# Kernel optimization log

Hardware: AMD Instinct MI355X
Metric: run time of the kernel (lower is better)

## Reference

```python
import jax, jax.numpy as jnp
import numpy as np

NEG_INF = -1.0e9
LEAKY_SLOPE = 0.2


def setup_inputs() -> dict:
    key = jax.random.key(0)
    ks = jax.random.split(key, 8)
    B, H, N, D = 4, 8, 256, 64
    query = jax.random.normal(ks[0], (B, H, N, D), dtype=jnp.float32)
    k_ = jax.random.normal(ks[1], (B, H, N, D), dtype=jnp.float32)
    value = jax.random.normal(ks[2], (B, H, N, D), dtype=jnp.float32)
    mask = jax.random.randint(ks[3], (B, 1, N, N), 0, 2, dtype=jnp.int32)
    # nn.Linear(d_k*2, d_k): weight (D, 2D), bias (D,)
    lim_h = 1.0 / np.sqrt(2 * D)
    W_h = jax.random.uniform(ks[4], (D, 2 * D), minval=-lim_h, maxval=lim_h, dtype=jnp.float32)
    b_h = jax.random.uniform(ks[5], (D,), minval=-lim_h, maxval=lim_h, dtype=jnp.float32)
    # nn.Linear(d_k, 1): weight (1, D), bias (1,)
    lim_o = 1.0 / np.sqrt(D)
    W_o = jax.random.uniform(ks[6], (1, D), minval=-lim_o, maxval=lim_o, dtype=jnp.float32)
    b_o = jax.random.uniform(ks[7], (1,), minval=-lim_o, maxval=lim_o, dtype=jnp.float32)
    return {"query": query, "key": k_, "value": value, "mask": mask,
            "W_h": W_h, "b_h": b_h, "W_o": W_o, "b_o": b_o}


def reference(query, key, value, mask, W_h, b_h, W_o, b_o):
    # W_h acts on concat([q, k]); decompose into two projections (same math):
    # W_h @ [q; k] = q @ W_q^T + k @ W_k^T
    D = query.shape[-1]
    Wq, Wk = W_h[:, :D], W_h[:, D:]
    q_proj = jnp.einsum('bhnd,ed->bhne', query, Wq)  # (B,H,N,D)
    k_proj = jnp.einsum('bhmd,ed->bhme', key, Wk)    # (B,H,N,D)
    # pairwise hidden: (B,H,N,N,D)
    hidden = q_proj[:, :, :, None, :] + k_proj[:, :, None, :, :] + b_h
    hidden = jax.nn.leaky_relu(hidden, negative_slope=LEAKY_SLOPE)
    scores = jnp.einsum('bhnme,e->bhnm', hidden, W_o[0]) + b_o[0]  # (B,H,N,N)
    scores = jnp.where(mask == 0, NEG_INF, scores)
    p_attn = jax.nn.softmax(scores, axis=-1)
    out = jnp.einsum('bhnm,bhmd->bhnd', p_attn, value)
    return out, p_attn
```

## Files before the change

kernel.cpp:

```cpp
#include <hip/hip_runtime.h>

constexpr int B = 4, H = 8, N = 256, D = 64;
constexpr int QBLK = 8;
constexpr int PATTN_OFF = B * H * N * D;
constexpr int NROWS = B * H * N;


__global__ __launch_bounds__(256) void proj_kernel(
    const float* __restrict__ q, const float* __restrict__ k,
    const float* __restrict__ W_h, const float* __restrict__ b_h,
    const float* __restrict__ W_o, const float* __restrict__ b_o,
    float* __restrict__ qp, float* __restrict__ kpb,
    float* __restrict__ cq6, float* __restrict__ ck6, float* __restrict__ w4)
{
    __shared__ float WT[128 * 65];
    int t = threadIdx.x;
    int lane = t & 63;
    int wid = __builtin_amdgcn_readfirstlane(t >> 6);
    int bid = blockIdx.x;
    int work = (bid & 7) * 32 + (bid >> 3);

    #pragma unroll
    for (int i = 0; i < 8; ++i) {
        int fidx = (t + i * 256) * 4;
        float4 w = *reinterpret_cast<const float4*>(W_h + fidx);
        int e = fidx >> 7, d = fidx & 127;
        WT[(d + 0) * 65 + e] = w.x;
        WT[(d + 1) * 65 + e] = w.y;
        WT[(d + 2) * 65 + e] = w.z;
        WT[(d + 3) * 65 + e] = w.w;
    }
    if (bid == 0 && t < 64) w4[t] = 0.4f * W_o[t];
    __syncthreads();

    int rbase = work * 32 + wid * 8;
    float accq[8] = {}, acck[8] = {};
    #pragma unroll
    for (int d0 = 0; d0 < 64; d0 += 16) {
        float wq[16], wk[16];
        #pragma unroll
        for (int d = 0; d < 16; ++d) {
            wq[d] = WT[(d0 + d) * 65 + lane];
            wk[d] = WT[(64 + d0 + d) * 65 + lane];
        }
        #pragma unroll
        for (int j = 0; j < 8; ++j) {
            const float* qrow = q + (rbase + j) * 64 + d0;
            const float* krow = k + (rbase + j) * 64 + d0;
            #pragma unroll
            for (int d = 0; d < 16; ++d) {
                accq[j] = fmaf(qrow[d], wq[d], accq[j]);
                acck[j] = fmaf(krow[d], wk[d], acck[j]);
            }
        }
    }
    float bh_e = b_h[lane];
    float wo = W_o[lane];
    float bo = b_o[0];
    #pragma unroll
    for (int j = 0; j < 8; ++j) {
        float aq = accq[j];
        float ak = acck[j] + bh_e;
        qp[(rbase + j) * 64 + lane] = aq;
        kpb[(rbase + j) * 64 + lane] = ak;
        float sq = wo * aq, sk = wo * ak;
        #pragma unroll
        for (int off = 32; off > 0; off >>= 1) {
            sq += __shfl_xor(sq, off, 64);
            sk += __shfl_xor(sk, off, 64);
        }
        if (lane == 0) {
            cq6[rbase + j] = 0.6f * sq + bo;
            ck6[rbase + j] = 0.6f * sk;
        }
    }
}

__global__ __launch_bounds__(512, 2) void attn_kernel(
    const float* __restrict__ qp, const float* __restrict__ kpb,
    const float* __restrict__ V, const int* __restrict__ mask,
    const float* __restrict__ cq6, const float* __restrict__ ck6,
    const float* __restrict__ w4g,
    float* __restrict__ out)
{
    __shared__ float smem[6144];
    __shared__ float red_s[8][4];

    int t = threadIdx.x;
    int lane = t & 63;
    int wid = __builtin_amdgcn_readfirstlane(t >> 6);
    int h = wid >> 2;
    int m = t & 255;
    int bid = blockIdx.x;
    int work = (bid & 7) * 128 + (bid >> 3);
    int bh = work >> 5;
    int nb = work & 31;
    int b = bh >> 3;
    int n0 = nb * QBLK;
    int kvbase = bh * N * 64;

    const float4* kp4 = reinterpret_cast<const float4*>(kpb + kvbase + m * 64 + h * 32);
    float4 c0 = kp4[0], c1 = kp4[1];

    float mf[4];
    #pragma unroll
    for (int i = 0; i < 4; ++i)
        mf[i] = (mask[(b * N + n0 + h * 4 + i) * N + m] != 0) ? 1.0f : 0.0f;

    float ckt = (h == 0) ? ck6[bh * N + m] : 0.f;

    float sp[8];
    const float* cq = cq6 + bh * N + n0;
    #pragma unroll
    for (int r = 0; r < 8; ++r) sp[r] = (h == 0) ? (cq[r] + ckt) : 0.f;

    const float* qr  = qp + (bh * N + n0) * 64 + h * 32;
    const float* w4h = w4g + h * 32;
    #pragma unroll
    for (int chunk = 0; chunk < 4; ++chunk) {
        float4 p0, p1;
        if (chunk < 3) { p0 = kp4[2 * chunk + 2]; p1 = kp4[2 * chunk + 3]; }
        float kvv[8] = {c0.x, c0.y, c0.z, c0.w, c1.x, c1.y, c1.z, c1.w};
        const float* qrc = qr + chunk * 8;
        const float* w4c = w4h + chunk * 8;
        #pragma unroll
        for (int e1 = 0; e1 < 8; ++e1) {
            float kve = kvv[e1];
            float we = w4c[e1];
            #pragma unroll
            for (int r = 0; r < 8; ++r)
                sp[r] = fmaf(we, fabsf(qrc[r * 64 + e1] + kve), sp[r]);
        }
        c0 = p0; c1 = p1;
    }
    #pragma unroll
    for (int r = 0; r < 8; ++r)
        smem[h * 2048 + r * 256 + m] = sp[r];

    const float* Vp = V + kvbase + wid * 32 * 64 + lane;
    float vpre0 = Vp[0 * 64], vpre1 = Vp[1 * 64], vpre2 = Vp[2 * 64], vpre3 = Vp[3 * 64];
    __syncthreads();

    float p8[4];
    #pragma unroll
    for (int i = 0; i < 4; ++i) {
        int rr = h * 4 + i;
        float s = smem[rr * 256 + m] + smem[2048 + rr * 256 + m];
        float p = __expf(s) * mf[i];
        p8[i] = p;
        float l = p;
        #pragma unroll
        for (int off = 32; off > 0; off >>= 1) l += __shfl_xor(l, off, 64);
        if (lane == 0) red_s[wid][i] = l;
    }
    __syncthreads();

    #pragma unroll
    for (int i = 0; i < 4; ++i) {
        int rr = h * 4 + i;
        float gs = red_s[h*4+0][i] + red_s[h*4+1][i] + red_s[h*4+2][i] + red_s[h*4+3][i];
        float pn = p8[i] * __frcp_rn(gs);
        smem[rr * 256 + m] = pn;
        out[PATTN_OFF + (bh * N + n0 + rr) * N + m] = pn;
    }
    __syncthreads();

    float acc[8] = {};
    {
        #pragma unroll
        for (int r = 0; r < 8; ++r) {
            float4 p4 = *reinterpret_cast<const float4*>(&smem[r * 256 + wid * 32]);
            acc[r] = fmaf(p4.x, vpre0, fmaf(p4.y, vpre1, fmaf(p4.z, vpre2, fmaf(p4.w, vpre3, acc[r]))));
        }
    }
    #pragma unroll
    for (int j = 4; j < 32; j += 4) {
        float v0 = Vp[(j+0) * 64];
        float v1 = Vp[(j+1) * 64];
        float v2 = Vp[(j+2) * 64];
        float v3 = Vp[(j+3) * 64];
        #pragma unroll
        for (int r = 0; r < 8; ++r) {
            float4 p4 = *reinterpret_cast<const float4*>(&smem[r * 256 + wid * 32 + j]);
            acc[r] = fmaf(p4.x, v0, fmaf(p4.y, v1, fmaf(p4.z, v2, fmaf(p4.w, v3, acc[r]))));
        }
    }
    #pragma unroll
    for (int r = 0; r < 8; ++r)
        smem[2048 + wid * 512 + r * 64 + lane] = acc[r];
    __syncthreads();

    float o = 0.f;
    #pragma unroll
    for (int mc = 0; mc < 8; ++mc)
        o += smem[2048 + mc * 512 + wid * 64 + lane];
    out[(bh * N + n0 + wid) * 64 + lane] = o;
}

extern "C" void kernel_launch(void* const* d_in, const int* in_sizes, int n_in,
                              void* d_out, int out_size, void* d_ws, size_t ws_size,
                              hipStream_t stream) {
    const float* q    = (const float*)d_in[0];
    const float* k    = (const float*)d_in[1];
    const float* v    = (const float*)d_in[2];
    const int*   mask = (const int*)d_in[3];
    const float* W_h  = (const float*)d_in[4];
    const float* b_h  = (const float*)d_in[5];
    const float* W_o  = (const float*)d_in[6];
    const float* b_o  = (const float*)d_in[7];
    float* out = (float*)d_out;

    float* qp  = (float*)d_ws;
    float* kpb = qp + NROWS * 64;
    float* cq6 = kpb + NROWS * 64;
    float* ck6 = cq6 + NROWS;
    float* w4  = ck6 + NROWS;

    proj_kernel<<<NROWS / 32, 256, 0, stream>>>(q, k, W_h, b_h, W_o, b_o, qp, kpb, cq6, ck6, w4);
    attn_kernel<<<B * H * (N / QBLK), 512, 0, stream>>>(qp, kpb, v, mask, cq6, ck6, w4, out);
}
```

Measured before the change: 39.16 us.

## Broadcast probabilities via readlane for PV instead of shared-memory staging

The P·V stage now keeps each wave's normalized probabilities in registers and broadcasts them with readlane. It drops the shared-memory write of probabilities and one block barrier. Each wave now covers its 4 query rows over a 64-key chunk, and a single reduction of 4 partials per output replaces the previous reduction of 8. The cost is 256 scalar readlanes per wave, each with a VALU-to-SALU dependency, and each wave reads twice as many V rows.

```diff
diff --git a/kernel.cpp b/kernel.cpp
--- a/kernel.cpp
+++ b/kernel.cpp
@@ -4,6 +4,10 @@
 constexpr int QBLK = 8;
 constexpr int PATTN_OFF = B * H * N * D;
 constexpr int NROWS = B * H * N;
+
+__device__ inline float readlane_f(float v, int l) {
+    return __builtin_bit_cast(float, __builtin_amdgcn_readlane(__builtin_bit_cast(int, v), l));
+}
 
 
 __global__ __launch_bounds__(256) void proj_kernel(
@@ -83,13 +87,15 @@
     const float* __restrict__ w4g,
     float* __restrict__ out)
 {
-    __shared__ float smem[6144];
+    __shared__ float sc[4096];
+    __shared__ float pv_s[2048];
     __shared__ float red_s[8][4];
 
     int t = threadIdx.x;
     int lane = t & 63;
     int wid = __builtin_amdgcn_readfirstlane(t >> 6);
     int h = wid >> 2;
+    int c = wid & 3;
     int m = t & 255;
     int bid = blockIdx.x;
     int work = (bid & 7) * 128 + (bid >> 3);
@@ -135,17 +141,17 @@
     }
     #pragma unroll
     for (int r = 0; r < 8; ++r)
-        smem[h * 2048 + r * 256 + m] = sp[r];
-
-    const float* Vp = V + kvbase + wid * 32 * 64 + lane;
-    float vpre0 = Vp[0 * 64], vpre1 = Vp[1 * 64], vpre2 = Vp[2 * 64], vpre3 = Vp[3 * 64];
+        sc[h * 2048 + r * 256 + m] = sp[r];
+
+    const float* Vw = V + kvbase + (c * 64) * 64 + lane;
+    float vpre0 = Vw[0 * 64], vpre1 = Vw[1 * 64], vpre2 = Vw[2 * 64], vpre3 = Vw[3 * 64];
     __syncthreads();
 
     float p8[4];
     #pragma unroll
     for (int i = 0; i < 4; ++i) {
         int rr = h * 4 + i;
-        float s = smem[rr * 256 + m] + smem[2048 + rr * 256 + m];
+        float s = sc[rr * 256 + m] + sc[2048 + rr * 256 + m];
         float p = __expf(s) * mf[i];
         p8[i] = p;
         float l = p;
@@ -155,46 +161,48 @@
     }
     __syncthreads();
 
+    float pn[4];
     #pragma unroll
     for (int i = 0; i < 4; ++i) {
         int rr = h * 4 + i;
         float gs = red_s[h*4+0][i] + red_s[h*4+1][i] + red_s[h*4+2][i] + red_s[h*4+3][i];
-        float pn = p8[i] * __frcp_rn(gs);
-        smem[rr * 256 + m] = pn;
-        out[PATTN_OFF + (bh * N + n0 + rr) * N + m] = pn;
-    }
-    __syncthreads();
-
-    float acc[8] = {};
+        pn[i] = p8[i] * __frcp_rn(gs);
+        out[PATTN_OFF + (bh * N + n0 + rr) * N + m] = pn[i];
+    }
+
+    float acc[4] = {};
     {
         #pragma unroll
-        for (int r = 0; r < 8; ++r) {
-            float4 p4 = *reinterpret_cast<const float4*>(&smem[r * 256 + wid * 32]);
-            acc[r] = fmaf(p4.x, vpre0, fmaf(p4.y, vpre1, fmaf(p4.z, vpre2, fmaf(p4.w, vpre3, acc[r]))));
-        }
-    }
-    #pragma unroll
-    for (int j = 4; j < 32; j += 4) {
-        float v0 = Vp[(j+0) * 64];
-        float v1 = Vp[(j+1) * 64];
-        float v2 = Vp[(j+2) * 64];
-        float v3 = Vp[(j+3) * 64];
-        #pragma unroll
-        for (int r = 0; r < 8; ++r) {
-            float4 p4 = *reinterpret_cast<const float4*>(&smem[r * 256 + wid * 32 + j]);
-            acc[r] = fmaf(p4.x, v0, fmaf(p4.y, v1, fmaf(p4.z, v2, fmaf(p4.w, v3, acc[r]))));
-        }
-    }
-    #pragma unroll
-    for (int r = 0; r < 8; ++r)
-        smem[2048 + wid * 512 + r * 64 + lane] = acc[r];
-    __syncthreads();
-
-    float o = 0.f;
-    #pragma unroll
-    for (int mc = 0; mc < 8; ++mc)
-        o += smem[2048 + mc * 512 + wid * 64 + lane];
-    out[(bh * N + n0 + wid) * 64 + lane] = o;
+        for (int i = 0; i < 4; ++i) {
+            acc[i] = fmaf(readlane_f(pn[i], 0), vpre0, acc[i]);
+            acc[i] = fmaf(readlane_f(pn[i], 1), vpre1, acc[i]);
+            acc[i] = fmaf(readlane_f(pn[i], 2), vpre2, acc[i]);
+            acc[i] = fmaf(readlane_f(pn[i], 3), vpre3, acc[i]);
+        }
+    }
+    #pragma unroll
+    for (int g = 1; g < 16; ++g) {
+        float v0 = Vw[(4*g+0) * 64];
+        float v1 = Vw[(4*g+1) * 64];
+        float v2 = Vw[(4*g+2) * 64];
+        float v3 = Vw[(4*g+3) * 64];
+        #pragma unroll
+        for (int i = 0; i < 4; ++i) {
+            acc[i] = fmaf(readlane_f(pn[i], 4*g+0), v0, acc[i]);
+            acc[i] = fmaf(readlane_f(pn[i], 4*g+1), v1, acc[i]);
+            acc[i] = fmaf(readlane_f(pn[i], 4*g+2), v2, acc[i]);
+            acc[i] = fmaf(readlane_f(pn[i], 4*g+3), v3, acc[i]);
+        }
+    }
+    #pragma unroll
+    for (int i = 0; i < 4; ++i)
+        pv_s[((h * 4 + i) * 4 + c) * 64 + lane] = acc[i];
+    __syncthreads();
+
+    int rr = t >> 6, d = t & 63;
+    float o = pv_s[(rr * 4 + 0) * 64 + d] + pv_s[(rr * 4 + 1) * 64 + d]
+            + pv_s[(rr * 4 + 2) * 64 + d] + pv_s[(rr * 4 + 3) * 64 + d];
+    out[(bh * N + n0 + rr) * 64 + d] = o;
 }
 
 extern "C" void kernel_launch(void* const* d_in, const int* in_sizes, int n_in,
```

After: 43.08 us. 1.1x slower.
